# Kernel optimization log

Hardware: AMD Instinct MI355X
Metric: run time of the kernel (lower is better)

Reference implementation:

```python
import jax, jax.numpy as jnp
import numpy as np

N = 160000   # total nodes
G = 800      # total graphs (B * 50)
NPG = 200    # nodes per graph
E = 1280000  # total edges (avg degree 8)
B = 16       # proteins
K = 2        # TAGConv hops
IN_F = 31
HID = 64


def setup_inputs() -> dict:
    key = jax.random.key(0)
    ks = jax.random.split(key, 16)
    s = 0.1
    x = jax.random.normal(ks[0], (N, IN_F), jnp.float32)
    src = jax.random.randint(ks[1], (E,), 0, N, jnp.int32)
    dst = jax.random.randint(ks[2], (E,), 0, N, jnp.int32)
    node2graph = jnp.repeat(jnp.arange(G, dtype=jnp.int32), NPG)
    W0 = jax.random.normal(ks[3], (IN_F * (K + 1), HID), jnp.float32) * s
    b0 = jax.random.normal(ks[4], (HID,), jnp.float32) * s
    W1 = jax.random.normal(ks[5], (HID * (K + 1), HID), jnp.float32) * s
    b1 = jax.random.normal(ks[6], (HID,), jnp.float32) * s
    W2 = jax.random.normal(ks[7], (HID * (K + 1), HID), jnp.float32) * s
    b2 = jax.random.normal(ks[8], (HID,), jnp.float32) * s
    W3 = jax.random.normal(ks[9], (HID * (K + 1), HID), jnp.float32) * s
    b3 = jax.random.normal(ks[10], (HID,), jnp.float32) * s
    Wg = jax.random.normal(ks[11], (HID, 1), jnp.float32) * s
    bg = jax.random.normal(ks[12], (1,), jnp.float32) * s
    return dict(x=x, src=src, dst=dst, node2graph=node2graph,
                W0=W0, b0=b0, W1=W1, b1=b1, W2=W2, b2=b2, W3=W3, b3=b3,
                Wg=Wg, bg=bg)


def reference(x, src, dst, node2graph, W0, b0, W1, b1, W2, b2, W3, b3, Wg, bg):
    # symmetric normalization: norm = in_degree^{-1/2}, clamped at 1 (DGL TAGConv)
    deg = jax.ops.segment_sum(jnp.ones((E,), x.dtype), dst, num_segments=N)
    norm = jax.lax.rsqrt(jnp.clip(deg, 1.0))[:, None]  # [N,1]

    def tag_conv(h, W, b):
        hops = [h]
        for _ in range(K):
            h = norm * jax.ops.segment_sum((h * norm)[src], dst, num_segments=N)
            hops.append(h)
        return jnp.concatenate(hops, axis=-1) @ W + b

    h = x
    for W, b in ((W0, b0), (W1, b1), (W2, b2), (W3, b3)):
        h = jax.nn.relu(tag_conv(h, W, b))

    # GlobalAttentionPooling: per-graph softmax over gate logits, weighted sum
    gate = h @ Wg + bg  # [N,1]
    gmax = jax.ops.segment_max(gate, node2graph, num_segments=G)  # [G,1]
    e = jnp.exp(gate - gmax[node2graph])
    z = jax.ops.segment_sum(e, node2graph, num_segments=G)
    alpha = e / z[node2graph]
    readout = jax.ops.segment_sum(alpha * h, node2graph, num_segments=G)  # [G,64]
    return readout.reshape(B, 50, HID)
```

## Files before the change

kernel.cpp:

```cpp
#include <hip/hip_runtime.h>

#define NN 160000
#define NE 1280000
#define NG 800
#define NPGR 200
#define INF_ 31
#define HID 64

typedef unsigned short bfu;
typedef __attribute__((ext_vector_type(8))) short short8;
typedef __attribute__((ext_vector_type(4))) float f32x4;

__device__ inline float bflo(unsigned u) { return __uint_as_float(u << 16); }
__device__ inline float bfhi(unsigned u) { return __uint_as_float(u & 0xffff0000u); }
__device__ inline float bfs(bfu s) { return __uint_as_float(((unsigned)s) << 16); }
__device__ inline unsigned f2bf(float x) {
  unsigned u = __float_as_uint(x);
  return (u + 0x7fffu + ((u >> 16) & 1u)) >> 16;
}
__device__ inline unsigned pack2(float a, float b) {
  return f2bf(a) | (f2bf(b) << 16);
}
__device__ inline void unpack8(uint4 v, float* f) {
  f[0] = bflo(v.x); f[1] = bfhi(v.x);
  f[2] = bflo(v.y); f[3] = bfhi(v.y);
  f[4] = bflo(v.z); f[5] = bfhi(v.z);
  f[6] = bflo(v.w); f[7] = bfhi(v.w);
}

__global__ __launch_bounds__(256) void k_izero(int* __restrict__ p, int n) {
  int i = blockIdx.x * 256 + threadIdx.x;
  if (i < n) p[i] = 0;
}

__global__ __launch_bounds__(256) void k_deg(const int* __restrict__ dst,
                                             int* __restrict__ deg, int E) {
  int e = blockIdx.x * 256 + threadIdx.x;
  if (e < E) atomicAdd(&deg[dst[e]], 1);
}

__global__ __launch_bounds__(256) void k_norm(const int* __restrict__ deg,
                                              float* __restrict__ norm, int n) {
  int i = blockIdx.x * 256 + threadIdx.x;
  if (i < n) norm[i] = rsqrtf(fmaxf((float)deg[i], 1.0f));
}

__global__ __launch_bounds__(256) void k_pad(const float* __restrict__ x,
                                             bfu* __restrict__ xb) {
  int i = blockIdx.x * 256 + threadIdx.x;
  int n = i >> 5, f = i & 31;
  float v = (f < INF_) ? x[(size_t)n * INF_ + f] : 0.f;
  xb[i] = (bfu)f2bf(v);
}

__global__ __launch_bounds__(256) void k_wfrag(const float* __restrict__ W,
                                               short* __restrict__ Wf) {
  int idx = blockIdx.x * 256 + threadIdx.x;
  int lane = idx & 63, t = (idx >> 6) & 3, step = idx >> 8;
  int col = t * 16 + (lane & 15);
  int kbase = step * 32 + ((lane >> 4) & 3) * 8;
  short8 o;
#pragma unroll
  for (int j = 0; j < 8; ++j)
    o[j] = (short)f2bf(W[(size_t)(kbase + j) * 64 + col]);
  *reinterpret_cast<short8*>(&Wf[(size_t)idx * 8]) = o;
}

__global__ __launch_bounds__(256) void k_wfrag0(const float* __restrict__ W0,
                                                short* __restrict__ Wf) {
  int idx = blockIdx.x * 256 + threadIdx.x;
  int lane = idx & 63, t = (idx >> 6) & 3, step = idx >> 8;
  int col = t * 16 + (lane & 15);
  int kbase = step * 32 + ((lane >> 4) & 3) * 8;
  short8 o;
#pragma unroll
  for (int j = 0; j < 8; ++j) {
    int r = kbase + j, pp = r >> 5, ir = r & 31;
    float v = (ir < INF_) ? W0[(size_t)(pp * INF_ + ir) * 64 + col] : 0.f;
    o[j] = (short)f2bf(v);
  }
  *reinterpret_cast<short8*>(&Wf[(size_t)idx * 8]) = o;
}

__global__ __launch_bounds__(256) void k_scan1(const int* __restrict__ in,
    int* __restrict__ out, int* __restrict__ bsum, int n) {
  __shared__ int sh[256];
  int tid = threadIdx.x;
  int base = blockIdx.x * 1024 + tid * 4;
  int v0 = (base + 0 < n) ? in[base + 0] : 0;
  int v1 = (base + 1 < n) ? in[base + 1] : 0;
  int v2 = (base + 2 < n) ? in[base + 2] : 0;
  int v3 = (base + 3 < n) ? in[base + 3] : 0;
  int t0 = v0, t1 = t0 + v1, t2 = t1 + v2, t3 = t2 + v3;
  sh[tid] = t3;
  __syncthreads();
  for (int off = 1; off < 256; off <<= 1) {
    int x = (tid >= off) ? sh[tid - off] : 0;
    __syncthreads();
    sh[tid] += x;
    __syncthreads();
  }
  int excl = (tid > 0) ? sh[tid - 1] : 0;
  if (base + 0 < n) out[base + 0] = excl;
  if (base + 1 < n) out[base + 1] = excl + t0;
  if (base + 2 < n) out[base + 2] = excl + t1;
  if (base + 3 < n) out[base + 3] = excl + t2;
  if (bsum && tid == 255) bsum[blockIdx.x] = sh[255];
}

__global__ __launch_bounds__(256) void k_scanadd(const int* __restrict__ part,
    const int* __restrict__ boff, int* __restrict__ rp,
    int* __restrict__ cursor, int n, int Etot) {
  int i = blockIdx.x * 256 + threadIdx.x;
  if (i < n) {
    int v = part[i] + boff[i >> 10];
    rp[i] = v;
    cursor[i] = v;
    if (i == 0) rp[n] = Etot;
  }
}

__global__ __launch_bounds__(256) void k_fill(const int* __restrict__ src,
    const int* __restrict__ dst, const float* __restrict__ norm,
    int* __restrict__ cursor, uint2* __restrict__ csr, int E) {
  int e = blockIdx.x * 256 + threadIdx.x;
  if (e < E) {
    int s = src[e];
    int p = atomicAdd(&cursor[dst[e]], 1);
    csr[p] = make_uint2((unsigned)s, __float_as_uint(norm[s]));
  }
}

template<int F>
__global__ __launch_bounds__(256) void k_gather(const bfu* __restrict__ hin,
    const int* __restrict__ rp, const uint2* __restrict__ csr,
    const float* __restrict__ norm, bfu* __restrict__ hout) {
  constexpr int LPN = F / 8;
  constexpr int NPB = 256 / LPN;
  int slot = threadIdx.x / LPN;
  int f8 = (threadIdx.x % LPN) * 8;
  int nid = blockIdx.x * NPB + slot;
  int beg = rp[nid], end = rp[nid + 1];
  float acc[8] = {0.f, 0.f, 0.f, 0.f, 0.f, 0.f, 0.f, 0.f};
  int e = beg;
  for (; e + 8 <= end; e += 8) {
    uint2 ed[8];
    uint4 v[8];
#pragma unroll
    for (int k = 0; k < 8; ++k) ed[k] = csr[e + k];
#pragma unroll
    for (int k = 0; k < 8; ++k)
      v[k] = *reinterpret_cast<const uint4*>(&hin[(size_t)ed[k].x * F + f8]);
#pragma unroll
    for (int k = 0; k < 8; ++k) {
      float f[8];
      unpack8(v[k], f);
      float w = __uint_as_float(ed[k].y);
#pragma unroll
      for (int q = 0; q < 8; ++q) acc[q] = fmaf(f[q], w, acc[q]);
    }
  }
  for (; e + 2 <= end; e += 2) {
    uint2 e0 = csr[e], e1 = csr[e + 1];
    uint4 v0 = *reinterpret_cast<const uint4*>(&hin[(size_t)e0.x * F + f8]);
    uint4 v1 = *reinterpret_cast<const uint4*>(&hin[(size_t)e1.x * F + f8]);
    float f0[8], f1[8];
    unpack8(v0, f0); unpack8(v1, f1);
    float w0 = __uint_as_float(e0.y), w1 = __uint_as_float(e1.y);
#pragma unroll
    for (int q = 0; q < 8; ++q) {
      acc[q] = fmaf(f0[q], w0, acc[q]);
      acc[q] = fmaf(f1[q], w1, acc[q]);
    }
  }
  if (e < end) {
    uint2 e0 = csr[e];
    uint4 v0 = *reinterpret_cast<const uint4*>(&hin[(size_t)e0.x * F + f8]);
    float f0[8];
    unpack8(v0, f0);
    float w0 = __uint_as_float(e0.y);
#pragma unroll
    for (int q = 0; q < 8; ++q) acc[q] = fmaf(f0[q], w0, acc[q]);
  }
  float wn = norm[nid];
#pragma unroll
  for (int q = 0; q < 8; ++q) acc[q] *= wn;
  uint4 o;
  o.x = pack2(acc[0], acc[1]);
  o.y = pack2(acc[2], acc[3]);
  o.z = pack2(acc[4], acc[5]);
  o.w = pack2(acc[6], acc[7]);
  *reinterpret_cast<uint4*>(&hout[(size_t)nid * F + f8]) = o;
}

template<int F>
__global__ __launch_bounds__(256) void k_gemm_mfma(const bfu* __restrict__ h0,
    const bfu* __restrict__ h1, const bfu* __restrict__ h2,
    const short* __restrict__ Wf, const float* __restrict__ bias,
    bfu* __restrict__ outb) {
  constexpr int SPP = F / 32;
  int wave = threadIdx.x >> 6, lane = threadIdx.x & 63;
  int quad = lane >> 4, l15 = lane & 15;
  int nb = blockIdx.x * 64 + wave * 16;

  f32x4 acc[4] = {{0.f,0.f,0.f,0.f}, {0.f,0.f,0.f,0.f},
                  {0.f,0.f,0.f,0.f}, {0.f,0.f,0.f,0.f}};
  const bfu* parts[3] = {h0, h1, h2};
#pragma unroll
  for (int p = 0; p < 3; ++p) {
    const bfu* __restrict__ P = parts[p] + (size_t)(nb + l15) * F + quad * 8;
#pragma unroll
    for (int s = 0; s < SPP; ++s) {
      short8 a = *reinterpret_cast<const short8*>(P + s * 32);
      int step = p * SPP + s;
      const short* __restrict__ wb = Wf + ((size_t)step * 4 * 64 + lane) * 8;
#pragma unroll
      for (int t = 0; t < 4; ++t) {
        short8 b = *reinterpret_cast<const short8*>(wb + (size_t)t * 64 * 8);
        acc[t] = __builtin_amdgcn_mfma_f32_16x16x32_bf16(a, b, acc[t], 0, 0, 0);
      }
    }
  }
#pragma unroll
  for (int t = 0; t < 4; ++t) {
    int col = t * 16 + l15;
    float bj = bias[col];
#pragma unroll
    for (int r = 0; r < 4; ++r) {
      int node = nb + quad * 4 + r;
      float v = fmaxf(acc[t][r] + bj, 0.f);
      outb[(size_t)node * 64 + col] = (bfu)f2bf(v);
    }
  }
}

__global__ __launch_bounds__(256) void k_pool(const bfu* __restrict__ h,
    const float* __restrict__ Wg, const float* __restrict__ bg,
    float* __restrict__ out) {
  int g = blockIdx.x;
  int tid = threadIdx.x;
  int lane = tid & 63, w = tid >> 6;
  const bfu* hg = h + (size_t)g * NPGR * HID;
  float wgt = Wg[lane];
  __shared__ float sgate[NPGR];
  __shared__ float sred[256];
  __shared__ float spart[4][64];

  for (int n = w; n < NPGR; n += 4) {
    float v = bfs(hg[(size_t)n * HID + lane]) * wgt;
    for (int off = 32; off > 0; off >>= 1) v += __shfl_down(v, off, 64);
    if (lane == 0) sgate[n] = v + bg[0];
  }
  __syncthreads();

  float m = -INFINITY;
  for (int n = tid; n < NPGR; n += 256) m = fmaxf(m, sgate[n]);
  sred[tid] = m;
  __syncthreads();
  for (int s = 128; s > 0; s >>= 1) {
    if (tid < s) sred[tid] = fmaxf(sred[tid], sred[tid + s]);
    __syncthreads();
  }
  float gmax = sred[0];
  __syncthreads();

  float zp = 0.f;
  for (int n = tid; n < NPGR; n += 256) {
    float e = expf(sgate[n] - gmax);
    sgate[n] = e;
    zp += e;
  }
  sred[tid] = zp;
  __syncthreads();
  for (int s = 128; s > 0; s >>= 1) {
    if (tid < s) sred[tid] += sred[tid + s];
    __syncthreads();
  }
  float z = sred[0];
  __syncthreads();

  float acc = 0.f;
  for (int n = w; n < NPGR; n += 4)
    acc += sgate[n] * bfs(hg[(size_t)n * HID + lane]);
  spart[w][lane] = acc;
  __syncthreads();
  if (w == 0) {
    float t = spart[0][lane] + spart[1][lane] + spart[2][lane] + spart[3][lane];
    out[(size_t)g * HID + lane] = t / z;
  }
}

extern "C" void kernel_launch(void* const* d_in, const int* in_sizes, int n_in,
                              void* d_out, int out_size, void* d_ws, size_t ws_size,
                              hipStream_t stream) {
  const float* x   = (const float*)d_in[0];
  const int*   src = (const int*)d_in[1];
  const int*   dst = (const int*)d_in[2];
  const float* W0 = (const float*)d_in[4];
  const float* b0 = (const float*)d_in[5];
  const float* W1 = (const float*)d_in[6];
  const float* b1 = (const float*)d_in[7];
  const float* W2 = (const float*)d_in[8];
  const float* b2 = (const float*)d_in[9];
  const float* W3 = (const float*)d_in[10];
  const float* b3 = (const float*)d_in[11];
  const float* Wg = (const float*)d_in[12];
  const float* bg = (const float*)d_in[13];
  float* out = (float*)d_out;

  const int N = NN, E = NE;
  const int NB1 = (N + 1023) / 1024;

  char* p = (char*)d_ws;
  uint2* csr  = (uint2*)p;           p += sizeof(uint2) * (size_t)E;
  int* deg     = (int*)p;            p += sizeof(int) * (size_t)N;
  int* part    = (int*)p;            p += sizeof(int) * (size_t)N;
  int* rp      = (int*)p;            p += sizeof(int) * (size_t)(N + 4);
  int* cursor  = (int*)p;            p += sizeof(int) * (size_t)N;
  int* bsum    = (int*)p;            p += sizeof(int) * 256;
  int* boff    = (int*)p;            p += sizeof(int) * 256;
  float* nrm   = (float*)p;          p += sizeof(float) * (size_t)N;
  short* Wf0   = (short*)p;          p += sizeof(short) * 768 * 8;
  short* Wf1   = (short*)p;          p += sizeof(short) * 1536 * 8;
  short* Wf2   = (short*)p;          p += sizeof(short) * 1536 * 8;
  short* Wf3   = (short*)p;          p += sizeof(short) * 1536 * 8;
  bfu* xb      = (bfu*)p;            p += sizeof(bfu) * (size_t)N * 32;
  bfu* h1b     = (bfu*)p;            p += sizeof(bfu) * (size_t)N * HID;
  bfu* h2b     = (bfu*)p;            p += sizeof(bfu) * (size_t)N * HID;
  bfu* hAb     = (bfu*)p;            p += sizeof(bfu) * (size_t)N * HID;
  bfu* hBb     = (bfu*)p;            p += sizeof(bfu) * (size_t)N * HID;

  k_izero<<<(N + 255) / 256, 256, 0, stream>>>(deg, N);
  k_deg<<<(E + 255) / 256, 256, 0, stream>>>(dst, deg, E);
  k_norm<<<(N + 255) / 256, 256, 0, stream>>>(deg, nrm, N);
  k_scan1<<<NB1, 256, 0, stream>>>(deg, part, bsum, N);
  k_scan1<<<1, 256, 0, stream>>>(bsum, boff, nullptr, NB1);
  k_scanadd<<<(N + 255) / 256, 256, 0, stream>>>(part, boff, rp, cursor, N, E);
  k_fill<<<(E + 255) / 256, 256, 0, stream>>>(src, dst, nrm, cursor, csr, E);

  k_pad<<<(N * 32) / 256, 256, 0, stream>>>(x, xb);
  k_wfrag0<<<3, 256, 0, stream>>>(W0, Wf0);
  k_wfrag<<<6, 256, 0, stream>>>(W1, Wf1);
  k_wfrag<<<6, 256, 0, stream>>>(W2, Wf2);
  k_wfrag<<<6, 256, 0, stream>>>(W3, Wf3);

  k_gather<32><<<N / 64, 256, 0, stream>>>(xb, rp, csr, nrm, h1b);
  k_gather<32><<<N / 64, 256, 0, stream>>>(h1b, rp, csr, nrm, h2b);
  k_gemm_mfma<32><<<N / 64, 256, 0, stream>>>(xb, h1b, h2b, Wf0, b0, hAb);

  const short* Wfs[3] = {Wf1, Wf2, Wf3};
  const float* bs[3] = {b1, b2, b3};
  bfu* hin = hAb;
  bfu* hout = hBb;
  for (int l = 0; l < 3; ++l) {
    k_gather<64><<<N / 32, 256, 0, stream>>>(hin, rp, csr, nrm, h1b);
    k_gather<64><<<N / 32, 256, 0, stream>>>(h1b, rp, csr, nrm, h2b);
    k_gemm_mfma<64><<<N / 64, 256, 0, stream>>>(hin, h1b, h2b, Wfs[l], bs[l], hout);
    bfu* t = hin; hin = hout; hout = t;
  }

  k_pool<<<NG, 256, 0, stream>>>(hin, Wg, bg, out);
}
```

Before: 688.0 us.

## Build CSR via two-pass bucketed scatter and degree-sort gather node order

Replaces the per-edge global atomic CSR fill with a two-pass build: edges are first binned into 256 destination-range buckets through shared-memory staging, then each bucket is scattered with LDS cursors, so the CSR writes become local. It also counting-sorts nodes by in-degree (capped at 63) into an order array, and the gather kernels process nodes in that order so warps see balanced edge counts. This adds several small kernels and reuses the hBb buffer as bucket scratch. It relies on a fixed per-bucket capacity of 6144 edges, which random inputs with mean 5000 should not exceed, and gather outputs are now accessed non-contiguously.

```diff
diff --git a/kernel.cpp b/kernel.cpp
--- a/kernel.cpp
+++ b/kernel.cpp
@@ -7,6 +7,11 @@
 #define INF_ 31
 #define HID 64
 
+#define NBUK 256
+#define NPBK 625
+#define BCAP 6144
+#define CHUNK 8192
+
 typedef unsigned short bfu;
 typedef __attribute__((ext_vector_type(8))) short short8;
 typedef __attribute__((ext_vector_type(4))) float f32x4;
@@ -39,10 +44,48 @@
   if (e < E) atomicAdd(&deg[dst[e]], 1);
 }
 
-__global__ __launch_bounds__(256) void k_norm(const int* __restrict__ deg,
-                                              float* __restrict__ norm, int n) {
-  int i = blockIdx.x * 256 + threadIdx.x;
-  if (i < n) norm[i] = rsqrtf(fmaxf((float)deg[i], 1.0f));
+__global__ __launch_bounds__(256) void k_normhist(const int* __restrict__ deg,
+    float* __restrict__ norm, int* __restrict__ hist, int n) {
+  __shared__ int h[64];
+  int tid = threadIdx.x;
+  if (tid < 64) h[tid] = 0;
+  __syncthreads();
+  int i = blockIdx.x * 256 + tid;
+  int bin = -1;
+  if (i < n) {
+    int d = deg[i];
+    norm[i] = rsqrtf(fmaxf((float)d, 1.0f));
+    bin = min(d, 63);
+    atomicAdd(&h[bin], 1);
+  }
+  __syncthreads();
+  if (tid < 64 && h[tid]) atomicAdd(&hist[tid], h[tid]);
+}
+
+__global__ __launch_bounds__(64) void k_dscan(const int* __restrict__ hist,
+                                              int* __restrict__ dcur) {
+  if (threadIdx.x == 0) {
+    int s = 0;
+    for (int i = 0; i < 64; ++i) { dcur[i] = s; s += hist[i]; }
+  }
+}
+
+__global__ __launch_bounds__(256) void k_dorder(const int* __restrict__ deg,
+    int* __restrict__ dcur, int* __restrict__ order, int n) {
+  __shared__ int cnt[64], gb[64];
+  int tid = threadIdx.x;
+  if (tid < 64) cnt[tid] = 0;
+  __syncthreads();
+  int i = blockIdx.x * 256 + tid;
+  int bin = -1, off = 0;
+  if (i < n) {
+    bin = min(deg[i], 63);
+    off = atomicAdd(&cnt[bin], 1);
+  }
+  __syncthreads();
+  if (tid < 64 && cnt[tid]) gb[tid] = atomicAdd(&dcur[tid], cnt[tid]);
+  __syncthreads();
+  if (i < n) order[gb[bin] + off] = i;
 }
 
 __global__ __launch_bounds__(256) void k_pad(const float* __restrict__ x,
@@ -109,37 +152,74 @@
 }
 
 __global__ __launch_bounds__(256) void k_scanadd(const int* __restrict__ part,
-    const int* __restrict__ boff, int* __restrict__ rp,
-    int* __restrict__ cursor, int n, int Etot) {
+    const int* __restrict__ boff, int* __restrict__ rp, int n, int Etot) {
   int i = blockIdx.x * 256 + threadIdx.x;
   if (i < n) {
-    int v = part[i] + boff[i >> 10];
-    rp[i] = v;
-    cursor[i] = v;
+    rp[i] = part[i] + boff[i >> 10];
     if (i == 0) rp[n] = Etot;
   }
 }
 
-__global__ __launch_bounds__(256) void k_fill(const int* __restrict__ src,
-    const int* __restrict__ dst, const float* __restrict__ norm,
-    int* __restrict__ cursor, uint2* __restrict__ csr, int E) {
-  int e = blockIdx.x * 256 + threadIdx.x;
-  if (e < E) {
-    int s = src[e];
-    int p = atomicAdd(&cursor[dst[e]], 1);
-    csr[p] = make_uint2((unsigned)s, __float_as_uint(norm[s]));
+__global__ __launch_bounds__(256) void k_gcinit(int* __restrict__ gcur) {
+  gcur[threadIdx.x] = threadIdx.x * BCAP;
+}
+
+__global__ __launch_bounds__(256) void k_bucket(const int* __restrict__ src,
+    const int* __restrict__ dst, int* __restrict__ gcur,
+    uint2* __restrict__ buk, int E) {
+  __shared__ uint2 stage[CHUNK];
+  __shared__ int cnt[NBUK], gbase[NBUK];
+  int tid = threadIdx.x;
+  int base = blockIdx.x * CHUNK;
+  int nch = min(CHUNK, E - base);
+  for (int i = tid; i < NBUK; i += 256) cnt[i] = 0;
+  __syncthreads();
+  for (int i = tid; i < nch; i += 256) {
+    int s = src[base + i], d = dst[base + i];
+    stage[i] = make_uint2((unsigned)s, (unsigned)d);
+    atomicAdd(&cnt[(unsigned)d / NPBK], 1);
+  }
+  __syncthreads();
+  for (int i = tid; i < NBUK; i += 256) {
+    gbase[i] = atomicAdd(&gcur[i], cnt[i]);
+    cnt[i] = 0;
+  }
+  __syncthreads();
+  for (int i = tid; i < nch; i += 256) {
+    uint2 r = stage[i];
+    int b = r.y / NPBK;
+    int off = atomicAdd(&cnt[b], 1);
+    buk[(size_t)gbase[b] + off] = r;
+  }
+}
+
+__global__ __launch_bounds__(256) void k_scat2(const uint2* __restrict__ buk,
+    const int* __restrict__ gcur, const int* __restrict__ rp,
+    const float* __restrict__ norm, uint2* __restrict__ csr) {
+  __shared__ int cur[NPBK];
+  int b = blockIdx.x, tid = threadIdx.x;
+  int nbase = b * NPBK;
+  for (int i = tid; i < NPBK; i += 256) cur[i] = rp[nbase + i];
+  __syncthreads();
+  int cnt = gcur[b] - b * BCAP;
+  const uint2* __restrict__ bp = buk + (size_t)b * BCAP;
+  for (int i = tid; i < cnt; i += 256) {
+    uint2 r = bp[i];
+    int pos = atomicAdd(&cur[r.y - nbase], 1);
+    csr[pos] = make_uint2(r.x, __float_as_uint(norm[r.x]));
   }
 }
 
 template<int F>
 __global__ __launch_bounds__(256) void k_gather(const bfu* __restrict__ hin,
     const int* __restrict__ rp, const uint2* __restrict__ csr,
-    const float* __restrict__ norm, bfu* __restrict__ hout) {
+    const float* __restrict__ norm, const int* __restrict__ order,
+    bfu* __restrict__ hout) {
   constexpr int LPN = F / 8;
   constexpr int NPB = 256 / LPN;
   int slot = threadIdx.x / LPN;
   int f8 = (threadIdx.x % LPN) * 8;
-  int nid = blockIdx.x * NPB + slot;
+  int nid = order[blockIdx.x * NPB + slot];
   int beg = rp[nid], end = rp[nid + 1];
   float acc[8] = {0.f, 0.f, 0.f, 0.f, 0.f, 0.f, 0.f, 0.f};
   int e = beg;
@@ -316,9 +396,12 @@
   int* deg     = (int*)p;            p += sizeof(int) * (size_t)N;
   int* part    = (int*)p;            p += sizeof(int) * (size_t)N;
   int* rp      = (int*)p;            p += sizeof(int) * (size_t)(N + 4);
-  int* cursor  = (int*)p;            p += sizeof(int) * (size_t)N;
+  int* order   = (int*)p;            p += sizeof(int) * (size_t)N;
   int* bsum    = (int*)p;            p += sizeof(int) * 256;
   int* boff    = (int*)p;            p += sizeof(int) * 256;
+  int* gcur    = (int*)p;            p += sizeof(int) * NBUK;
+  int* hist64  = (int*)p;            p += sizeof(int) * 64;
+  int* dcur    = (int*)p;            p += sizeof(int) * 64;
   float* nrm   = (float*)p;          p += sizeof(float) * (size_t)N;
   short* Wf0   = (short*)p;          p += sizeof(short) * 768 * 8;
   short* Wf1   = (short*)p;          p += sizeof(short) * 1536 * 8;
@@ -329,14 +412,20 @@
   bfu* h2b     = (bfu*)p;            p += sizeof(bfu) * (size_t)N * HID;
   bfu* hAb     = (bfu*)p;            p += sizeof(bfu) * (size_t)N * HID;
   bfu* hBb     = (bfu*)p;            p += sizeof(bfu) * (size_t)N * HID;
+  uint2* buk   = (uint2*)hBb;
 
   k_izero<<<(N + 255) / 256, 256, 0, stream>>>(deg, N);
+  k_izero<<<1, 256, 0, stream>>>(hist64, 64);
   k_deg<<<(E + 255) / 256, 256, 0, stream>>>(dst, deg, E);
-  k_norm<<<(N + 255) / 256, 256, 0, stream>>>(deg, nrm, N);
+  k_normhist<<<(N + 255) / 256, 256, 0, stream>>>(deg, nrm, hist64, N);
   k_scan1<<<NB1, 256, 0, stream>>>(deg, part, bsum, N);
   k_scan1<<<1, 256, 0, stream>>>(bsum, boff, nullptr, NB1);
-  k_scanadd<<<(N + 255) / 256, 256, 0, stream>>>(part, boff, rp, cursor, N, E);
-  k_fill<<<(E + 255) / 256, 256, 0, stream>>>(src, dst, nrm, cursor, csr, E);
+  k_scanadd<<<(N + 255) / 256, 256, 0, stream>>>(part, boff, rp, N, E);
+  k_gcinit<<<1, NBUK, 0, stream>>>(gcur);
+  k_bucket<<<(E + CHUNK - 1) / CHUNK, 256, 0, stream>>>(src, dst, gcur, buk, E);
+  k_scat2<<<NBUK, 256, 0, stream>>>(buk, gcur, rp, nrm, csr);
+  k_dscan<<<1, 64, 0, stream>>>(hist64, dcur);
+  k_dorder<<<(N + 255) / 256, 256, 0, stream>>>(deg, dcur, order, N);
 
   k_pad<<<(N * 32) / 256, 256, 0, stream>>>(x, xb);
   k_wfrag0<<<3, 256, 0, stream>>>(W0, Wf0);
@@ -344,8 +433,8 @@
   k_wfrag<<<6, 256, 0, stream>>>(W2, Wf2);
   k_wfrag<<<6, 256, 0, stream>>>(W3, Wf3);
 
-  k_gather<32><<<N / 64, 256, 0, stream>>>(xb, rp, csr, nrm, h1b);
-  k_gather<32><<<N / 64, 256, 0, stream>>>(h1b, rp, csr, nrm, h2b);
+  k_gather<32><<<N / 64, 256, 0, stream>>>(xb, rp, csr, nrm, order, h1b);
+  k_gather<32><<<N / 64, 256, 0, stream>>>(h1b, rp, csr, nrm, order, h2b);
   k_gemm_mfma<32><<<N / 64, 256, 0, stream>>>(xb, h1b, h2b, Wf0, b0, hAb);
 
   const short* Wfs[3] = {Wf1, Wf2, Wf3};
@@ -353,8 +442,8 @@
   bfu* hin = hAb;
   bfu* hout = hBb;
   for (int l = 0; l < 3; ++l) {
-    k_gather<64><<<N / 32, 256, 0, stream>>>(hin, rp, csr, nrm, h1b);
-    k_gather<64><<<N / 32, 256, 0, stream>>>(h1b, rp, csr, nrm, h2b);
+    k_gather<64><<<N / 32, 256, 0, stream>>>(hin, rp, csr, nrm, order, h1b);
+    k_gather<64><<<N / 32, 256, 0, stream>>>(h1b, rp, csr, nrm, order, h2b);
     k_gemm_mfma<64><<<N / 64, 256, 0, stream>>>(hin, h1b, h2b, Wfs[l], bs[l], hout);
     bfu* t = hin; hin = hout; hout = t;
   }
```

Result: slower. 734.7 us (+6.8%).
